# Kernel optimization log

Measured on AMD Instinct MI355X. Metric: run time of the kernel, lower is better.

## Reference

```python
import jax, jax.numpy as jnp
import numpy as np

B, H, S, D = 16, 12, 1024, 64  # batch, heads, seq, head_dim (dim=768, num_head=12)


def setup_inputs() -> dict:
    key = jax.random.key(0)
    ks = jax.random.split(key, 9)
    sc = 1.0 / np.sqrt(D)
    return {
        "x": jax.random.normal(ks[0], (B, H, S, D), dtype=jnp.float32),
        "Wq": jax.random.normal(ks[1], (D, D), dtype=jnp.float32) * sc,
        "bq": jax.random.normal(ks[2], (D,), dtype=jnp.float32) * 0.02,
        "Wk": jax.random.normal(ks[3], (D, D), dtype=jnp.float32) * sc,
        "bk": jax.random.normal(ks[4], (D,), dtype=jnp.float32) * 0.02,
        "Wv": jax.random.normal(ks[5], (D, D), dtype=jnp.float32) * sc,
        "bv": jax.random.normal(ks[6], (D,), dtype=jnp.float32) * 0.02,
        "Wo": jax.random.normal(ks[7], (D, D), dtype=jnp.float32) * sc,
        "bo": jax.random.normal(ks[8], (D,), dtype=jnp.float32) * 0.02,
    }


def reference(x, Wq, bq, Wk, bk, Wv, bv, Wo, bo):
    # torch Linear: y = x @ W^T + b, applied to last dim (head_dim)
    q = jnp.einsum("bhsd,ed->bhse", x, Wq) + bq
    k = jnp.einsum("bhsd,ed->bhse", x, Wk) + bk
    v = jnp.einsum("bhsd,ed->bhse", x, Wv) + bv
    scores = jnp.einsum("bhqd,bhkd->bhqk", q, k) / jnp.sqrt(jnp.float32(q.shape[-1]))
    attn = jax.nn.softmax(scores, axis=-1)
    out = jnp.einsum("bhqk,bhkd->bhqd", attn, v)
    out = jnp.einsum("bhsd,ed->bhse", out, Wo) + bo
    return out
```

## Files before the change

### kernel.cpp

```cpp
#include <hip/hip_runtime.h>
#include <math.h>


typedef __bf16 bf16x8 __attribute__((ext_vector_type(8)));
typedef float  f32x4  __attribute__((ext_vector_type(4)));

#define MFMA(a, b, c) __builtin_amdgcn_mfma_f32_16x16x32_bf16((a), (b), (c), 0, 0, 0)

static constexpr int S = 1024;
static constexpr int PAD = 72;
static constexpr size_t NE = 196608ull * 64ull;
static constexpr float QSCALE = 0.125f * 1.4426950408889634f;

__device__ inline unsigned long long pack4bf(float a, float b, float c, float d) {
    union { __bf16 h[4]; unsigned long long u; } pk;
    pk.h[0] = (__bf16)a; pk.h[1] = (__bf16)b; pk.h[2] = (__bf16)c; pk.h[3] = (__bf16)d;
    return pk.u;
}

__global__ void wo_conv(const float* __restrict__ Wo, __bf16* __restrict__ wob) {
    int i = (blockIdx.x * 256 + threadIdx.x) * 4;
    float4 v = *(const float4*)(Wo + i);
    *(unsigned long long*)(wob + i) = pack4bf(v.x, v.y, v.z, v.w);
}

__global__ __launch_bounds__(256) void proj_qkv(
    const float* __restrict__ x,
    const float* __restrict__ Wq, const float* __restrict__ bq,
    const float* __restrict__ Wk, const float* __restrict__ bk,
    const float* __restrict__ Wv, const float* __restrict__ bv,
    __bf16* __restrict__ gq, __bf16* __restrict__ gk, __bf16* __restrict__ gvt)
{
    __shared__ __align__(16) __bf16 lx[128][PAD];
    __shared__ __align__(16) __bf16 lw[3][64][PAD];
    __shared__ __align__(16) __bf16 lbuf[128][PAD];
    __shared__ float lb[3][64];

    const int tid = threadIdx.x;
    const int row_base = blockIdx.x * 128;

    #pragma unroll
    for (int i = tid * 4; i < 8192; i += 1024) {
        float4 v = *(const float4*)(x + (size_t)row_base * 64 + i);
        int r = i >> 6, c = i & 63;
        *(unsigned long long*)&lx[r][c] = pack4bf(v.x, v.y, v.z, v.w);
    }
    const float* Ws[3] = {Wq, Wk, Wv};
    #pragma unroll
    for (int mtx = 0; mtx < 3; mtx++) {
        #pragma unroll
        for (int i = tid * 4; i < 4096; i += 1024) {
            float4 v = *(const float4*)(Ws[mtx] + i);
            int r = i >> 6, c = i & 63;
            *(unsigned long long*)&lw[mtx][r][c] = pack4bf(v.x, v.y, v.z, v.w);
        }
    }
    if (tid < 64) { lb[0][tid] = bq[tid]; lb[1][tid] = bk[tid]; lb[2][tid] = bv[tid]; }
    __syncthreads();

    const int w = tid >> 6, lane = tid & 63, m = lane & 15, quad = lane >> 4;
    const int bh = row_base >> 10;
    const int s_base = row_base & 1023;

    bf16x8 xf[2][2];
    #pragma unroll
    for (int g = 0; g < 2; g++) {
        xf[g][0] = *(const bf16x8*)&lx[w * 32 + g * 16 + m][quad * 8];
        xf[g][1] = *(const bf16x8*)&lx[w * 32 + g * 16 + m][32 + quad * 8];
    }

    #pragma unroll
    for (int mtx = 0; mtx < 2; mtx++) {
        #pragma unroll
        for (int et = 0; et < 4; et++) {
            bf16x8 wf0 = *(const bf16x8*)&lw[mtx][et * 16 + m][quad * 8];
            bf16x8 wf1 = *(const bf16x8*)&lw[mtx][et * 16 + m][32 + quad * 8];
            float4 bias = *(const float4*)&lb[mtx][et * 16 + quad * 4];
            #pragma unroll
            for (int g = 0; g < 2; g++) {
                f32x4 acc = {0.f, 0.f, 0.f, 0.f};
                acc = MFMA(wf0, xf[g][0], acc);
                acc = MFMA(wf1, xf[g][1], acc);
                unsigned long long u;
                if (mtx == 0)
                    u = pack4bf((acc[0] + bias.x) * QSCALE, (acc[1] + bias.y) * QSCALE,
                                (acc[2] + bias.z) * QSCALE, (acc[3] + bias.w) * QSCALE);
                else
                    u = pack4bf(acc[0] + bias.x, acc[1] + bias.y,
                                acc[2] + bias.z, acc[3] + bias.w);
                *(unsigned long long*)&lbuf[w * 32 + g * 16 + m][et * 16 + quad * 4] = u;
            }
        }
        __syncthreads();
        __bf16* dst = (mtx == 0 ? gq : gk);
        #pragma unroll
        for (int it = 0; it < 4; it++) {
            int idx = it * 256 + tid;
            int row = idx >> 3, col = (idx & 7) * 8;
            *(uint4*)(dst + ((size_t)row_base + row) * 64 + col) = *(uint4*)&lbuf[row][col];
        }
        __syncthreads();
    }

    __bf16 (*lvt)[136] = (__bf16(*)[136])&lbuf[0][0];
    #pragma unroll
    for (int et = 0; et < 4; et++) {
        bf16x8 wf0 = *(const bf16x8*)&lw[2][et * 16 + m][quad * 8];
        bf16x8 wf1 = *(const bf16x8*)&lw[2][et * 16 + m][32 + quad * 8];
        const float bias = lb[2][et * 16 + m];
        #pragma unroll
        for (int g = 0; g < 2; g++) {
            f32x4 acc = {0.f, 0.f, 0.f, 0.f};
            acc = MFMA(xf[g][0], wf0, acc);
            acc = MFMA(xf[g][1], wf1, acc);
            *(unsigned long long*)&lvt[et * 16 + m][w * 32 + g * 16 + quad * 4] =
                pack4bf(acc[0] + bias, acc[1] + bias, acc[2] + bias, acc[3] + bias);
        }
    }
    __syncthreads();
    #pragma unroll
    for (int it = 0; it < 4; it++) {
        int idx = it * 256 + tid;
        int row = idx >> 4, col = (idx & 15) * 8;
        *(uint4*)(gvt + ((size_t)bh * 64 + row) * 1024 + s_base + col) = *(uint4*)&lvt[row][col];
    }
}

__global__ __launch_bounds__(256) void attn(
    const __bf16* __restrict__ gq, const __bf16* __restrict__ gk,
    const __bf16* __restrict__ gvt, const __bf16* __restrict__ wob,
    const float* __restrict__ bo, float* __restrict__ out)
{
    __shared__ __align__(16) __bf16 lk[64][PAD];
    __shared__ __align__(16) __bf16 lv[64][PAD];
    __shared__ __align__(16) __bf16 lp[4][64][PAD];

    const int tid = threadIdx.x;
    const int w = tid >> 6, lane = tid & 63, m = lane & 15, quad = lane >> 4;
    const int bh = blockIdx.x;
    const int q0 = blockIdx.y * 256 + w * 64;

    bf16x8 qf[4][2];
    #pragma unroll
    for (int g = 0; g < 4; g++) {
        const __bf16* qrow = gq + ((size_t)bh * S + q0 + g * 16 + m) * 64;
        qf[g][0] = *(const bf16x8*)(qrow + quad * 8);
        qf[g][1] = *(const bf16x8*)(qrow + 32 + quad * 8);
    }

    f32x4 o[4][4];
    float lsum[4] = {0.f, 0.f, 0.f, 0.f};
    #pragma unroll
    for (int g = 0; g < 4; g++)
        #pragma unroll
        for (int n = 0; n < 4; n++) o[g][n] = {0.f, 0.f, 0.f, 0.f};

    const int sr = tid >> 3;
    const int sc = (tid & 7) * 8;
    const __bf16* kbase = gk + (size_t)bh * S * 64;
    const __bf16* vbase = gvt + (size_t)bh * 64 * 1024;

    uint4 kreg0 = *(const uint4*)(kbase + (size_t)sr * 64 + sc);
    uint4 kreg1 = *(const uint4*)(kbase + (size_t)(sr + 32) * 64 + sc);
    uint4 vreg0 = *(const uint4*)(vbase + (size_t)sr * 1024 + sc);
    uint4 vreg1 = *(const uint4*)(vbase + (size_t)(sr + 32) * 1024 + sc);

    for (int kb = 0; kb < 16; kb++) {
        __syncthreads();
        *(uint4*)&lk[sr][sc]      = kreg0;
        *(uint4*)&lk[sr + 32][sc] = kreg1;
        *(uint4*)&lv[sr][sc]      = vreg0;
        *(uint4*)&lv[sr + 32][sc] = vreg1;
        if (kb < 15) {
            const int nb = (kb + 1) * 64;
            kreg0 = *(const uint4*)(kbase + (size_t)(nb + sr) * 64 + sc);
            kreg1 = *(const uint4*)(kbase + (size_t)(nb + sr + 32) * 64 + sc);
            vreg0 = *(const uint4*)(vbase + (size_t)sr * 1024 + nb + sc);
            vreg1 = *(const uint4*)(vbase + (size_t)(sr + 32) * 1024 + nb + sc);
        }
        __syncthreads();

        #pragma unroll
        for (int t = 0; t < 4; t++) {
            bf16x8 ka0 = *(const bf16x8*)&lk[t * 16 + m][quad * 8];
            bf16x8 ka1 = *(const bf16x8*)&lk[t * 16 + m][32 + quad * 8];
            #pragma unroll
            for (int g = 0; g < 4; g++) {
                f32x4 acc = {0.f, 0.f, 0.f, 0.f};
                acc = MFMA(ka0, qf[g][0], acc);
                acc = MFMA(ka1, qf[g][1], acc);
                float e0 = __builtin_exp2f(acc[0]), e1 = __builtin_exp2f(acc[1]);
                float e2 = __builtin_exp2f(acc[2]), e3 = __builtin_exp2f(acc[3]);
                lsum[g] += (e0 + e1) + (e2 + e3);
                *(unsigned long long*)&lp[w][g * 16 + m][t * 16 + quad * 4] =
                    pack4bf(e0, e1, e2, e3);
            }
        }

        bf16x8 pb[4][2];
        #pragma unroll
        for (int g = 0; g < 4; g++) {
            pb[g][0] = *(const bf16x8*)&lp[w][g * 16 + m][quad * 8];
            pb[g][1] = *(const bf16x8*)&lp[w][g * 16 + m][32 + quad * 8];
        }
        #pragma unroll
        for (int n = 0; n < 4; n++) {
            bf16x8 va0 = *(const bf16x8*)&lv[n * 16 + m][quad * 8];
            bf16x8 va1 = *(const bf16x8*)&lv[n * 16 + m][32 + quad * 8];
            #pragma unroll
            for (int g = 0; g < 4; g++) {
                o[g][n] = MFMA(va0, pb[g][0], o[g][n]);
                o[g][n] = MFMA(va1, pb[g][1], o[g][n]);
            }
        }
    }

    #pragma unroll
    for (int g = 0; g < 4; g++) {
        lsum[g] += __shfl_xor(lsum[g], 16);
        lsum[g] += __shfl_xor(lsum[g], 32);
        const float inv = 1.f / lsum[g];
        #pragma unroll
        for (int n = 0; n < 4; n++) {
            *(unsigned long long*)&lp[w][g * 16 + m][n * 16 + quad * 4] =
                pack4bf(o[g][n][0] * inv, o[g][n][1] * inv,
                        o[g][n][2] * inv, o[g][n][3] * inv);
        }
    }

    bf16x8 wf[4][2];
    #pragma unroll
    for (int et = 0; et < 4; et++) {
        wf[et][0] = *(const bf16x8*)(wob + (size_t)(et * 16 + m) * 64 + quad * 8);
        wf[et][1] = *(const bf16x8*)(wob + (size_t)(et * 16 + m) * 64 + 32 + quad * 8);
    }
    float biasr[4];
    #pragma unroll
    for (int et = 0; et < 4; et++) biasr[et] = bo[et * 16 + m];

    #pragma unroll
    for (int g = 0; g < 4; g++) {
        bf16x8 af0 = *(const bf16x8*)&lp[w][g * 16 + m][quad * 8];
        bf16x8 af1 = *(const bf16x8*)&lp[w][g * 16 + m][32 + quad * 8];
        #pragma unroll
        for (int et = 0; et < 4; et++) {
            f32x4 acc = {0.f, 0.f, 0.f, 0.f};
            acc = MFMA(af0, wf[et][0], acc);
            acc = MFMA(af1, wf[et][1], acc);
            #pragma unroll
            for (int r = 0; r < 4; r++) {
                size_t row = (size_t)bh * S + q0 + g * 16 + quad * 4 + r;
                out[row * 64 + et * 16 + m] = acc[r] + biasr[et];
            }
        }
    }
}

extern "C" void kernel_launch(void* const* d_in, const int* in_sizes, int n_in,
                              void* d_out, int out_size, void* d_ws, size_t ws_size,
                              hipStream_t stream) {
    const float* x  = (const float*)d_in[0];
    const float* Wq = (const float*)d_in[1];
    const float* bq = (const float*)d_in[2];
    const float* Wk = (const float*)d_in[3];
    const float* bk = (const float*)d_in[4];
    const float* Wv = (const float*)d_in[5];
    const float* bv = (const float*)d_in[6];
    const float* Wo = (const float*)d_in[7];
    const float* bo = (const float*)d_in[8];
    float* out = (float*)d_out;

    __bf16* gq  = (__bf16*)d_ws;
    __bf16* gk  = gq + NE;
    __bf16* gvt = gk + NE;
    __bf16* wob = gvt + NE;

    wo_conv<<<4, 256, 0, stream>>>(Wo, wob);
    proj_qkv<<<1536, 256, 0, stream>>>(x, Wq, bq, Wk, bk, Wv, bv, gq, gk, gvt);
    attn<<<dim3(192, 4), 256, 0, stream>>>(gq, gk, gvt, wob, bo, out);
}
```

Before: 227.5 us.

## Load K/V MFMA fragments directly from global into registers, drop LDS staging

The attention kernel no longer stages K and V tiles through shared memory with two block barriers per key block. Each wave now loads its MFMA fragments for K and V^T straight from global memory (L2-cached), prefetching the next K block into registers. This removes the per-iteration __syncthreads and the LDS traffic. It also switches exp2 to the raw hardware intrinsic and sets a minimum of 3 blocks per SM in launch bounds. The cost is redundant global loads: every wave reads the same K/V data, which relies on cache hits, and register pressure rises.

```diff
diff --git a/kernel.cpp b/kernel.cpp
--- a/kernel.cpp
+++ b/kernel.cpp
@@ -126,13 +126,11 @@
     }
 }
 
-__global__ __launch_bounds__(256) void attn(
+__global__ __launch_bounds__(256, 3) void attn(
     const __bf16* __restrict__ gq, const __bf16* __restrict__ gk,
     const __bf16* __restrict__ gvt, const __bf16* __restrict__ wob,
     const float* __restrict__ bo, float* __restrict__ out)
 {
-    __shared__ __align__(16) __bf16 lk[64][PAD];
-    __shared__ __align__(16) __bf16 lv[64][PAD];
     __shared__ __align__(16) __bf16 lp[4][64][PAD];
 
     const int tid = threadIdx.x;
@@ -140,6 +138,9 @@
     const int bh = blockIdx.x;
     const int q0 = blockIdx.y * 256 + w * 64;
 
+    const __bf16* kbase = gk + (size_t)bh * S * 64;
+    const __bf16* vbase = gvt + (size_t)bh * 64 * 1024;
+
     bf16x8 qf[4][2];
     #pragma unroll
     for (int g = 0; g < 4; g++) {
@@ -155,42 +156,34 @@
         #pragma unroll
         for (int n = 0; n < 4; n++) o[g][n] = {0.f, 0.f, 0.f, 0.f};
 
-    const int sr = tid >> 3;
-    const int sc = (tid & 7) * 8;
-    const __bf16* kbase = gk + (size_t)bh * S * 64;
-    const __bf16* vbase = gvt + (size_t)bh * 64 * 1024;
-
-    uint4 kreg0 = *(const uint4*)(kbase + (size_t)sr * 64 + sc);
-    uint4 kreg1 = *(const uint4*)(kbase + (size_t)(sr + 32) * 64 + sc);
-    uint4 vreg0 = *(const uint4*)(vbase + (size_t)sr * 1024 + sc);
-    uint4 vreg1 = *(const uint4*)(vbase + (size_t)(sr + 32) * 1024 + sc);
+    bf16x8 ka[4][2];
+    #pragma unroll
+    for (int t = 0; t < 4; t++) {
+        const __bf16* kr = kbase + (size_t)(t * 16 + m) * 64;
+        ka[t][0] = *(const bf16x8*)(kr + quad * 8);
+        ka[t][1] = *(const bf16x8*)(kr + 32 + quad * 8);
+    }
 
     for (int kb = 0; kb < 16; kb++) {
-        __syncthreads();
-        *(uint4*)&lk[sr][sc]      = kreg0;
-        *(uint4*)&lk[sr + 32][sc] = kreg1;
-        *(uint4*)&lv[sr][sc]      = vreg0;
-        *(uint4*)&lv[sr + 32][sc] = vreg1;
-        if (kb < 15) {
-            const int nb = (kb + 1) * 64;
-            kreg0 = *(const uint4*)(kbase + (size_t)(nb + sr) * 64 + sc);
-            kreg1 = *(const uint4*)(kbase + (size_t)(nb + sr + 32) * 64 + sc);
-            vreg0 = *(const uint4*)(vbase + (size_t)sr * 1024 + nb + sc);
-            vreg1 = *(const uint4*)(vbase + (size_t)(sr + 32) * 1024 + nb + sc);
-        }
-        __syncthreads();
+        bf16x8 va[4][2];
+        #pragma unroll
+        for (int n = 0; n < 4; n++) {
+            const __bf16* vr = vbase + (size_t)(n * 16 + m) * 1024 + kb * 64;
+            va[n][0] = *(const bf16x8*)(vr + quad * 8);
+            va[n][1] = *(const bf16x8*)(vr + 32 + quad * 8);
+        }
 
         #pragma unroll
         for (int t = 0; t < 4; t++) {
-            bf16x8 ka0 = *(const bf16x8*)&lk[t * 16 + m][quad * 8];
-            bf16x8 ka1 = *(const bf16x8*)&lk[t * 16 + m][32 + quad * 8];
             #pragma unroll
             for (int g = 0; g < 4; g++) {
                 f32x4 acc = {0.f, 0.f, 0.f, 0.f};
-                acc = MFMA(ka0, qf[g][0], acc);
-                acc = MFMA(ka1, qf[g][1], acc);
-                float e0 = __builtin_exp2f(acc[0]), e1 = __builtin_exp2f(acc[1]);
-                float e2 = __builtin_exp2f(acc[2]), e3 = __builtin_exp2f(acc[3]);
+                acc = MFMA(ka[t][0], qf[g][0], acc);
+                acc = MFMA(ka[t][1], qf[g][1], acc);
+                float e0 = __builtin_amdgcn_exp2f(acc[0]);
+                float e1 = __builtin_amdgcn_exp2f(acc[1]);
+                float e2 = __builtin_amdgcn_exp2f(acc[2]);
+                float e3 = __builtin_amdgcn_exp2f(acc[3]);
                 lsum[g] += (e0 + e1) + (e2 + e3);
                 *(unsigned long long*)&lp[w][g * 16 + m][t * 16 + quad * 4] =
                     pack4bf(e0, e1, e2, e3);
@@ -203,14 +196,22 @@
             pb[g][0] = *(const bf16x8*)&lp[w][g * 16 + m][quad * 8];
             pb[g][1] = *(const bf16x8*)&lp[w][g * 16 + m][32 + quad * 8];
         }
+
+        if (kb < 15) {
+            #pragma unroll
+            for (int t = 0; t < 4; t++) {
+                const __bf16* kr = kbase + (size_t)((kb + 1) * 64 + t * 16 + m) * 64;
+                ka[t][0] = *(const bf16x8*)(kr + quad * 8);
+                ka[t][1] = *(const bf16x8*)(kr + 32 + quad * 8);
+            }
+        }
+
         #pragma unroll
         for (int n = 0; n < 4; n++) {
-            bf16x8 va0 = *(const bf16x8*)&lv[n * 16 + m][quad * 8];
-            bf16x8 va1 = *(const bf16x8*)&lv[n * 16 + m][32 + quad * 8];
             #pragma unroll
             for (int g = 0; g < 4; g++) {
-                o[g][n] = MFMA(va0, pb[g][0], o[g][n]);
-                o[g][n] = MFMA(va1, pb[g][1], o[g][n]);
+                o[g][n] = MFMA(va[n][0], pb[g][0], o[g][n]);
+                o[g][n] = MFMA(va[n][1], pb[g][1], o[g][n]);
             }
         }
     }
```

After: 345.9 us. +52.0%, slower.
